# Kernel optimization log

Measured on AMD Instinct MI355X. Metric: run time of the kernel, lower is better.

## Reference

```python
import jax, jax.numpy as jnp
import numpy as np

B = 8          # batch_size
N = 2048       # N_particles
D_SP = 2       # spatial dims
D = 16         # D_SP + hidden_dim
K = 32         # max_num_neighbors
R = 0.08       # neighbor_radius
DT = 0.01      # leapfrog step
BIG = 1e9


def setup_inputs() -> dict:
    key = jax.random.key(0)
    ks = jax.random.split(key, 8)
    H, C = 64, 32
    # node state: small random hidden features, deterministic disk positions
    x = jax.random.normal(ks[0], (B * N, D), dtype=jnp.float32) * 0.001
    i = jnp.arange(N, dtype=jnp.float32)
    golden = jnp.pi * (3.0 - jnp.sqrt(5.0))
    theta = i * golden
    r = 0.6 * jnp.sqrt((i + 0.5) / N)
    pos = jnp.stack([r * jnp.cos(theta), r * jnp.sin(theta)], axis=1)  # [N,2]
    pos = jnp.tile(pos, (B, 1)) + 0.01 * jax.random.normal(ks[1], (B * N, 2), dtype=jnp.float32)
    x = x.at[:, :D_SP].set(pos)
    W1 = jax.random.normal(ks[2], (2 * D, H), dtype=jnp.float32) * (1.0 / np.sqrt(2 * D))
    b1 = jnp.zeros((H,), jnp.float32)
    W2 = jax.random.normal(ks[3], (H, C), dtype=jnp.float32) * (1.0 / np.sqrt(H))
    b2 = jnp.zeros((C,), jnp.float32)
    Wout = jax.random.normal(ks[4], (C, 1), dtype=jnp.float32) * (1.0 / np.sqrt(C))
    bout = jnp.zeros((1,), jnp.float32)
    batch = jnp.repeat(jnp.arange(B, dtype=jnp.int64), N)
    return {"x": x, "W1": W1, "b1": b1, "W2": W2, "b2": b2,
            "Wout": Wout, "bout": bout, "batch": batch, "steps": 2}


def reference(x, W1, b1, W2, b2, Wout, bout, batch, steps):
    Bn, Df = x.shape
    Bc = int(np.asarray(batch)[-1]) + 1      # batch is contiguous blocks
    Nn = Bn // Bc
    eye = jnp.eye(Nn, dtype=x.dtype) * BIG   # no self-loops (loop=False)

    def hamiltonian(xv):
        xb = xv.reshape(Bc, Nn, Df)
        pos = xb[:, :, :D_SP]                              # [B,N,2]
        # radius_graph: pairwise sq-dist per simulation, capped at K neighbors
        d2 = jnp.sum((pos[:, :, None, :] - pos[:, None, :, :]) ** 2, axis=-1)  # [B,N,N]
        d2 = d2 + eye
        negd, idx = jax.lax.top_k(-d2, K)                  # K nearest per node
        valid = (-negd) < (R * R)                          # [B,N,K]
        # gather neighbor states (HNNConv message on concat(x_i, x_j))
        xj = xb[jnp.arange(Bc)[:, None, None], idx]        # [B,N,K,D]
        xi = jnp.broadcast_to(xb[:, :, None, :], xj.shape)
        m = jnp.tanh(jnp.concatenate([xi, xj], axis=-1) @ W1 + b1)  # [B,N,K,H]
        m = m @ W2 + b2                                    # [B,N,K,C]
        m = jnp.where(valid[..., None], m, 0.0)
        agg = m.sum(axis=2)                                # sum aggregation [B,N,C]
        h = agg @ Wout + bout                              # per-node Hamiltonian [B,N,1]
        return h.sum()

    for _ in range(int(steps)):
        dHdx = jax.grad(hamiltonian)(x)
        x = x - DT * dHdx
    return x
```

## Files before the change

### kernel.cpp

```cpp
#include <hip/hip_runtime.h>
#include <cstdint>
#include <cstddef>

#define BB   8
#define NN   2048
#define DD   16
#define HHH  64
#define KK   32
#define CAP  96
#define FCAP 48
#define DT_C 0.01f
#define R2_C (0.08f * 0.08f)
#define CEXP (-2.885390081777927f)

#define BANDS    18
#define BAND_OFF 0.72f
#define BAND_INV 12.5f

#define WPB   8
#define BLOCK (WPB * 64)

__device__ __forceinline__ float dist2(float px, float py, float qx, float qy) {
    float dx = __fsub_rn(px, qx);
    float dy = __fsub_rn(py, qy);
    return __fadd_rn(__fmul_rn(dx, dx), __fmul_rn(dy, dy));
}

__device__ __forceinline__ int prefix_cnt(unsigned long long m) {
    return (int)__builtin_amdgcn_mbcnt_hi(
        (unsigned)(m >> 32), __builtin_amdgcn_mbcnt_lo((unsigned)m, 0u));
}

__device__ __forceinline__ int swizzled_particle(int blk, int w, int& bbase) {
    int vb = blk & 7, vi = blk >> 3;
    bbase = vb << 11;
    return bbase + vi * WPB + w;
}

template <bool FIRST>
__global__ __launch_bounds__(1024) void k_bin(
    const float* __restrict__ x, const float* __restrict__ pos,
    const float* __restrict__ W2, const float* __restrict__ Wout,
    float2* __restrict__ sortedPos, unsigned short* __restrict__ sortedIdx,
    int* __restrict__ bandStart, float* __restrict__ vOut) {
    __shared__ int hist[BANDS], base[BANDS + 1], cursor[BANDS];
    int bat = blockIdx.x;
    int bbase = bat << 11;
    int tid = threadIdx.x;
    if (tid < BANDS) hist[tid] = 0;
    if (blockIdx.x == 0 && tid >= 64 && tid < 64 + HHH) {
        int hh = tid - 64;
        float acc = 0.f;
        for (int c = 0; c < 32; c++) acc = fmaf(W2[hh * 32 + c], Wout[c], acc);
        vOut[hh] = acc;
    }
    __syncthreads();
    float2 q[2]; int bd[2];
#pragma unroll
    for (int u = 0; u < 2; ++u) {
        int i = tid + (u << 10);
        float2 qq;
        if (FIRST) qq = *(const float2*)(x + (size_t)(bbase + i) * DD);
        else       qq = *(const float2*)(pos + (size_t)(bbase + i) * 2);
        q[u] = qq;
        int band = (int)((qq.y + BAND_OFF) * BAND_INV);
        band = band < 0 ? 0 : (band > BANDS - 1 ? BANDS - 1 : band);
        bd[u] = band;
        atomicAdd(&hist[band], 1);
    }
    __syncthreads();
    if (tid == 0) {
        int acc = 0;
        for (int k = 0; k < BANDS; ++k) { base[k] = acc; cursor[k] = acc; acc += hist[k]; }
        base[BANDS] = acc;
    }
    __syncthreads();
    if (tid <= BANDS) bandStart[bat * 32 + tid] = base[tid];
#pragma unroll
    for (int u = 0; u < 2; ++u) {
        int i = tid + (u << 10);
        int dst = atomicAdd(&cursor[bd[u]], 1);
        sortedPos[bbase + dst] = q[u];
        sortedIdx[bbase + dst] = (unsigned short)i;
    }
}

__global__ __launch_bounds__(BLOCK) void k_neighbors(
    const float* __restrict__ x,
    const float2* __restrict__ sortedPos, const unsigned short* __restrict__ sortedIdx,
    const int* __restrict__ bandStart, const float* __restrict__ W1,
    float2* __restrict__ candList, unsigned short* __restrict__ fwdList,
    int* __restrict__ cntArr, float* __restrict__ cutArr,
    float* __restrict__ Aplane, float* __restrict__ Dplane) {
    __shared__ float2 sDJ[WPB][CAP];

    int tid = threadIdx.x;
    int w = tid >> 6, lane = tid & 63;
    int bbase;
    int p = swizzled_particle(blockIdx.x, w, bbase);
    int pl = p & (NN - 1);
    int bat = bbase >> 11;

    float xv = (lane < DD) ? x[(size_t)p * DD + lane] : 0.f;
    float px = __shfl(xv, 0), py = __shfl(xv, 1);
    float A = 0.f, Dv = 0.f;
#pragma unroll
    for (int f = 0; f < DD; f++) {
        float xf = __shfl(xv, f);
        A  = fmaf(xf, W1[f * HHH + lane], A);
        Dv = fmaf(xf, W1[(DD + f) * HHH + lane], Dv);
    }
    Aplane[((size_t)p << 6) + lane] = A;
    Dplane[((size_t)p << 6) + lane] = Dv;

    int bb = (int)((py + BAND_OFF) * BAND_INV);
    bb = bb < 0 ? 0 : (bb > BANDS - 1 ? BANDS - 1 : bb);
    int lo = bandStart[bat * 32 + (bb > 0 ? bb - 1 : 0)];
    int hi = bandStart[bat * 32 + (bb < BANDS - 1 ? bb + 2 : BANDS)];

    int cnt = 0;
    for (int c0 = lo; c0 < hi; c0 += 64) {
        int j = c0 + lane;
        float2 q = (j < hi) ? sortedPos[bbase + j] : make_float2(1e30f, 1e30f);
        float d2 = dist2(px, py, q.x, q.y);
        bool hit = (j < hi) && (d2 < R2_C);
        unsigned long long m = __ballot(hit);
        int idx = cnt + prefix_cnt(m);
        if (hit && idx < CAP)
            sDJ[w][idx] = make_float2(d2, __uint_as_float((unsigned)j));
        cnt += (int)__popcll(m);
    }
    if (cnt > CAP) cnt = CAP;
    __threadfence_block();

    float cutoff = R2_C;
    if (cnt > KK + 1) {
        const float INF = 1e30f;
        if (cnt <= 64) {
            float v = (lane < cnt) ? sDJ[w][lane].x : INF;
#pragma unroll
            for (int k = 2; k <= 64; k <<= 1) {
#pragma unroll
                for (int j = k >> 1; j > 0; j >>= 1) {
                    float pv = __shfl_xor(v, j);
                    bool up = ((lane & k) == 0);
                    bool takeMin = (((lane & j) == 0) == up);
                    v = takeMin ? fminf(v, pv) : fmaxf(v, pv);
                }
            }
            cutoff = __shfl(v, KK);
        } else {
            float e0 = (lane < cnt) ? sDJ[w][lane].x : INF;
            float e1 = (lane + 64 < cnt) ? sDJ[w][lane + 64].x : INF;
            int r0 = 0, q0 = 0, r1 = 0, q1 = 0;
            for (int k = 0; k < cnt; k++) {
                float val = sDJ[w][k].x;
                r0 += (val < e0); q0 += (val == e0);
                r1 += (val < e1); q1 += (val == e1);
            }
            bool c0 = (r0 <= KK) && (r0 + q0 > KK);
            bool c1 = (r1 <= KK) && (r1 + q1 > KK);
            float cand = c0 ? e0 : (c1 ? e1 : INF);
#pragma unroll
            for (int off = 32; off; off >>= 1) cand = fminf(cand, __shfl_xor(cand, off));
            cutoff = cand;
        }
    }

    int me = 0, mf = 0;
    for (int c0 = 0; c0 < cnt; c0 += 64) {
        int c = c0 + lane;
        bool act = c < cnt;
        float2 e = sDJ[w][act ? c : 0];
        unsigned js = __float_as_uint(e.y);
        int jo = act ? (int)sortedIdx[bbase + js] : pl;
        bool keep = act && (jo != pl);
        unsigned long long mK = __ballot(keep);
        int ie = me + prefix_cnt(mK);
        if (keep)
            candList[(size_t)p * CAP + ie] = make_float2(e.x, __uint_as_float((unsigned)jo));
        me += (int)__popcll(mK);
        bool fw = keep && (e.x <= cutoff);
        unsigned long long mF = __ballot(fw);
        int iF = mf + prefix_cnt(mF);
        if (fw && iF < FCAP) fwdList[(size_t)p * FCAP + iF] = (unsigned short)jo;
        mf += (int)__popcll(mF);
    }
    if (mf > FCAP) mf = FCAP;
    if (lane == 0) { cutArr[p] = cutoff; cntArr[p] = me | (mf << 16); }
}

__global__ __launch_bounds__(BLOCK) void k_grad(
    const float* __restrict__ x,
    const float* __restrict__ cutArr, const int* __restrict__ cntArr,
    const float2* __restrict__ candList, const unsigned short* __restrict__ fwdList,
    const float* __restrict__ Aplane, const float* __restrict__ Dplane,
    const float* __restrict__ W1, const float* __restrict__ b1,
    const float* __restrict__ vArr,
    float* __restrict__ xOut, float* __restrict__ posOut) {
    __shared__ float sW1t[HHH * 33];
    __shared__ alignas(16) unsigned short sFwd[WPB][FCAP];
    __shared__ alignas(16) unsigned short sRev[WPB][CAP];
    __shared__ float sS[WPB][128];

    int tid = threadIdx.x;
    int w = tid >> 6, h = tid & 63;
    int bbase;
    int p = swizzled_particle(blockIdx.x, w, bbase);

    for (int t = tid; t < 2 * DD * HHH; t += BLOCK) {
        int f = t >> 6, hh = t & 63;
        sW1t[hh * 33 + f] = W1[t];
    }
    __syncthreads();

    float b1h = b1[h];
    float Apb = Aplane[((size_t)p << 6) + h] + b1h;
    float Dpb = Dplane[((size_t)p << 6) + h] + b1h;
    float vh4 = 4.f * vArr[h];
    int packed = cntArr[p];
    int cnt = packed & 0xffff;
    int mf = packed >> 16;

    if (h < mf) sFwd[w][h] = fwdList[(size_t)p * FCAP + h];

    int mr = 0;
    for (int c0 = 0; c0 < cnt; c0 += 64) {
        int c = c0 + h;
        bool act = c < cnt;
        float2 e = candList[(size_t)p * CAP + (act ? c : 0)];
        unsigned jl = __float_as_uint(e.y) & (NN - 1);
        bool rev = act && (e.x <= cutArr[bbase + jl]);
        unsigned long long mR = __ballot(rev);
        int iR = mr + prefix_cnt(mR);
        if (rev) sRev[w][iR] = (unsigned short)jl;
        mr += (int)__popcll(mR);
    }
    __threadfence_block();

    const float* baseD = Dplane + ((size_t)bbase << 6);
    const float* baseA = Aplane + ((size_t)bbase << 6);
    float T1 = 0.f, T2 = 0.f;

    auto s2core = [&](float z) {
        float a = __builtin_amdgcn_exp2f(CEXP * fabsf(z));
        float bb = 1.f + a;
        return a * __builtin_amdgcn_rcpf(bb * bb);
    };

#define UNPACK8(Q0, Q1, U)                                            \
    unsigned U[8];                                                    \
    U[0] = (unsigned)__builtin_amdgcn_readfirstlane(Q0.x);            \
    U[1] = (unsigned)__builtin_amdgcn_readfirstlane(Q0.y);            \
    U[2] = (unsigned)__builtin_amdgcn_readfirstlane(Q0.z);            \
    U[3] = (unsigned)__builtin_amdgcn_readfirstlane(Q0.w);            \
    U[4] = (unsigned)__builtin_amdgcn_readfirstlane(Q1.x);            \
    U[5] = (unsigned)__builtin_amdgcn_readfirstlane(Q1.y);            \
    U[6] = (unsigned)__builtin_amdgcn_readfirstlane(Q1.z);            \
    U[7] = (unsigned)__builtin_amdgcn_readfirstlane(Q1.w);

    {
        const unsigned short* L = sFwd[w];
        int c = 0;
        for (; c + 16 <= mf; c += 16) {
            int4 q0 = *(const int4*)(L + c);
            int4 q1 = *(const int4*)(L + c + 8);
            UNPACK8(q0, q1, u)
            float d[16];
#pragma unroll
            for (int k = 0; k < 8; ++k) {
                d[2 * k]     = baseD[((size_t)(u[k] & 0xffffu) << 6) + h];
                d[2 * k + 1] = baseD[((size_t)(u[k] >> 16) << 6) + h];
            }
#pragma unroll
            for (int k = 0; k < 16; ++k) T1 += s2core(Apb + d[k]);
        }
        for (; c + 8 <= mf; c += 8) {
            int4 q0 = *(const int4*)(L + c);
            int4 q1 = q0;
            UNPACK8(q0, q1, u)
            float d[8];
#pragma unroll
            for (int k = 0; k < 4; ++k) {
                d[2 * k]     = baseD[((size_t)(u[k] & 0xffffu) << 6) + h];
                d[2 * k + 1] = baseD[((size_t)(u[k] >> 16) << 6) + h];
            }
#pragma unroll
            for (int k = 0; k < 8; ++k) T1 += s2core(Apb + d[k]);
        }
        for (; c < mf; ++c) {
            unsigned jl = (unsigned)__builtin_amdgcn_readfirstlane((int)L[c]);
            T1 += s2core(Apb + baseD[((size_t)jl << 6) + h]);
        }
    }
    {
        const unsigned short* L = sRev[w];
        int c = 0;
        for (; c + 16 <= mr; c += 16) {
            int4 q0 = *(const int4*)(L + c);
            int4 q1 = *(const int4*)(L + c + 8);
            UNPACK8(q0, q1, u)
            float d[16];
#pragma unroll
            for (int k = 0; k < 8; ++k) {
                d[2 * k]     = baseA[((size_t)(u[k] & 0xffffu) << 6) + h];
                d[2 * k + 1] = baseA[((size_t)(u[k] >> 16) << 6) + h];
            }
#pragma unroll
            for (int k = 0; k < 16; ++k) T2 += s2core(Dpb + d[k]);
        }
        for (; c + 8 <= mr; c += 8) {
            int4 q0 = *(const int4*)(L + c);
            int4 q1 = q0;
            UNPACK8(q0, q1, u)
            float d[8];
#pragma unroll
            for (int k = 0; k < 4; ++k) {
                d[2 * k]     = baseA[((size_t)(u[k] & 0xffffu) << 6) + h];
                d[2 * k + 1] = baseA[((size_t)(u[k] >> 16) << 6) + h];
            }
#pragma unroll
            for (int k = 0; k < 8; ++k) T2 += s2core(Dpb + d[k]);
        }
        for (; c < mr; ++c) {
            unsigned jl = (unsigned)__builtin_amdgcn_readfirstlane((int)L[c]);
            T2 += s2core(Dpb + baseA[((size_t)jl << 6) + h]);
        }
    }
#undef UNPACK8

    sS[w][h] = vh4 * T1;
    sS[w][64 + h] = vh4 * T2;
    __threadfence_block();

    float g = 0.f;
    if (h < 32) {
        const float* Sv = &sS[w][(h < 16) ? 0 : 64];
        float a0 = 0.f, a1 = 0.f, a2 = 0.f, a3 = 0.f;
        for (int hh = 0; hh < 64; hh += 4) {
            a0 = fmaf(sW1t[(hh + 0) * 33 + h], Sv[hh + 0], a0);
            a1 = fmaf(sW1t[(hh + 1) * 33 + h], Sv[hh + 1], a1);
            a2 = fmaf(sW1t[(hh + 2) * 33 + h], Sv[hh + 2], a2);
            a3 = fmaf(sW1t[(hh + 3) * 33 + h], Sv[hh + 3], a3);
        }
        g = (a0 + a1) + (a2 + a3);
    }
    float g2 = __shfl(g, (h + 16) & 63);
    if (h < DD) {
        float xn = x[(size_t)p * DD + h] - DT_C * (g + g2);
        xOut[(size_t)p * DD + h] = xn;
        if (h < 2) posOut[p * 2 + h] = xn;
    }
}

extern "C" void kernel_launch(void* const* d_in, const int* in_sizes, int n_in,
                              void* d_out, int out_size, void* d_ws, size_t ws_size,
                              hipStream_t stream) {
    const float* x0   = (const float*)d_in[0];
    const float* W1   = (const float*)d_in[1];
    const float* b1   = (const float*)d_in[2];
    const float* W2   = (const float*)d_in[3];
    const float* Wout = (const float*)d_in[5];
    float* out = (float*)d_out;

    float* ws   = (float*)d_ws;
    float* posA = ws;
    float* posB = posA + 32768;
    float* x1   = posB + 32768;
    float* Apl  = x1 + 262144;
    float* Dpl  = Apl + 16384 * 64;
    float* cut  = Dpl + 16384 * 64;
    int*   cnt  = (int*)(cut + 16384);
    float2* cand = (float2*)(cnt + 16384);
    unsigned short* fwd = (unsigned short*)(cand + (size_t)16384 * CAP);
    float2* sPosS = (float2*)(fwd + (size_t)16384 * FCAP);
    unsigned short* sIdx = (unsigned short*)(sPosS + 16384);
    int* bandStart = (int*)(sIdx + 16384);
    float* vArr = (float*)(bandStart + 8 * 32);

    const int NB = (BB * NN) / WPB;

    k_bin<true><<<BB, 1024, 0, stream>>>(x0, nullptr, W2, Wout, sPosS, sIdx,
                                         bandStart, vArr);
    k_neighbors<<<NB, BLOCK, 0, stream>>>(x0, sPosS, sIdx, bandStart, W1,
                                          cand, fwd, cnt, cut, Apl, Dpl);
    k_grad<<<NB, BLOCK, 0, stream>>>(x0, cut, cnt, cand, fwd, Apl, Dpl,
                                     W1, b1, vArr, x1, posB);
    k_bin<false><<<BB, 1024, 0, stream>>>(nullptr, posB, W2, Wout, sPosS, sIdx,
                                          bandStart, vArr);
    k_neighbors<<<NB, BLOCK, 0, stream>>>(x1, sPosS, sIdx, bandStart, W1,
                                          cand, fwd, cnt, cut, Apl, Dpl);
    k_grad<<<NB, BLOCK, 0, stream>>>(x1, cut, cnt, cand, fwd, Apl, Dpl,
                                     W1, b1, vArr, out, posA);
}
```

Baseline: 170.7 us.

## Replace 1D band binning with 2D cell grid and process particles in sorted order

The neighbor search now bins particles into a 17x17 uniform 2D grid instead of horizontal bands. Each particle scans only the three row-contiguous ranges covering its 3x3 cell neighborhood, which cuts the number of candidate distance tests. The cell histogram prefix sum becomes a warp-level scan. Per-particle work is also indexed by cell-sorted slot, so candidate and forward lists hold sorted indices and gathers of Aplane, Dplane and cutArr in the gradient kernel are spatially local. The cost is an extra sortedIdx indirection when reading x and writing the outputs, and a more complex candidate-index computation.

```diff
diff --git a/kernel.cpp b/kernel.cpp
--- a/kernel.cpp
+++ b/kernel.cpp
@@ -13,9 +13,11 @@
 #define R2_C (0.08f * 0.08f)
 #define CEXP (-2.885390081777927f)
 
-#define BANDS    18
-#define BAND_OFF 0.72f
-#define BAND_INV 12.5f
+#define GRID 17
+#define NCEL (GRID * GRID)
+#define GOFF 0.68f
+#define CINV 12.5f
+#define CSTRIDE 320
 
 #define WPB   8
 #define BLOCK (WPB * 64)
@@ -31,10 +33,13 @@
         (unsigned)(m >> 32), __builtin_amdgcn_mbcnt_lo((unsigned)m, 0u));
 }
 
-__device__ __forceinline__ int swizzled_particle(int blk, int w, int& bbase) {
-    int vb = blk & 7, vi = blk >> 3;
-    bbase = vb << 11;
-    return bbase + vi * WPB + w;
+__device__ __forceinline__ int swizzled_slot(int blk, int w, int& bbase) {
+    bbase = (blk & 7) << 11;
+    return (blk >> 3) * WPB + w;
+}
+
+__device__ __forceinline__ int clampi(int v, int lo, int hi) {
+    return v < lo ? lo : (v > hi ? hi : v);
 }
 
 template <bool FIRST>
@@ -42,53 +47,68 @@
     const float* __restrict__ x, const float* __restrict__ pos,
     const float* __restrict__ W2, const float* __restrict__ Wout,
     float2* __restrict__ sortedPos, unsigned short* __restrict__ sortedIdx,
-    int* __restrict__ bandStart, float* __restrict__ vOut) {
-    __shared__ int hist[BANDS], base[BANDS + 1], cursor[BANDS];
-    int bat = blockIdx.x;
-    int bbase = bat << 11;
-    int tid = threadIdx.x;
-    if (tid < BANDS) hist[tid] = 0;
-    if (blockIdx.x == 0 && tid >= 64 && tid < 64 + HHH) {
-        int hh = tid - 64;
+    int* __restrict__ cellStart, float* __restrict__ vOut) {
+    __shared__ int hist[NCEL], base[NCEL + 1], cursor[NCEL];
+    int bat = blockIdx.x, bbase = bat << 11, tid = threadIdx.x;
+    if (tid < NCEL) hist[tid] = 0;
+    if (blockIdx.x == 0 && tid >= 512 && tid < 512 + HHH) {
+        int hh = tid - 512;
         float acc = 0.f;
         for (int c = 0; c < 32; c++) acc = fmaf(W2[hh * 32 + c], Wout[c], acc);
         vOut[hh] = acc;
     }
     __syncthreads();
-    float2 q[2]; int bd[2];
+    float2 q[2]; int cid[2];
 #pragma unroll
     for (int u = 0; u < 2; ++u) {
         int i = tid + (u << 10);
-        float2 qq;
-        if (FIRST) qq = *(const float2*)(x + (size_t)(bbase + i) * DD);
-        else       qq = *(const float2*)(pos + (size_t)(bbase + i) * 2);
+        float2 qq = FIRST ? *(const float2*)(x + (size_t)(bbase + i) * DD)
+                          : *(const float2*)(pos + (size_t)(bbase + i) * 2);
         q[u] = qq;
-        int band = (int)((qq.y + BAND_OFF) * BAND_INV);
-        band = band < 0 ? 0 : (band > BANDS - 1 ? BANDS - 1 : band);
-        bd[u] = band;
-        atomicAdd(&hist[band], 1);
+        int cx = clampi((int)((qq.x + GOFF) * CINV), 0, GRID - 1);
+        int cy = clampi((int)((qq.y + GOFF) * CINV), 0, GRID - 1);
+        cid[u] = cy * GRID + cx;
+        atomicAdd(&hist[cid[u]], 1);
     }
     __syncthreads();
-    if (tid == 0) {
-        int acc = 0;
-        for (int k = 0; k < BANDS; ++k) { base[k] = acc; cursor[k] = acc; acc += hist[k]; }
-        base[BANDS] = acc;
+    if (tid < 64) {
+        int loc[5], s = 0;
+#pragma unroll
+        for (int k = 0; k < 5; ++k) {
+            int idx = tid * 5 + k;
+            loc[k] = (idx < NCEL) ? hist[idx] : 0;
+            s += loc[k];
+        }
+        int pre = s;
+#pragma unroll
+        for (int off = 1; off < 64; off <<= 1) {
+            int t = __shfl_up(pre, off);
+            if (tid >= off) pre += t;
+        }
+        pre -= s;
+#pragma unroll
+        for (int k = 0; k < 5; ++k) {
+            int idx = tid * 5 + k;
+            if (idx <= NCEL) base[idx] = pre;
+            pre += loc[k];
+        }
     }
     __syncthreads();
-    if (tid <= BANDS) bandStart[bat * 32 + tid] = base[tid];
+    if (tid < NCEL) cursor[tid] = base[tid];
+    if (tid <= NCEL) cellStart[bat * CSTRIDE + tid] = base[tid];
+    __syncthreads();
 #pragma unroll
     for (int u = 0; u < 2; ++u) {
-        int i = tid + (u << 10);
-        int dst = atomicAdd(&cursor[bd[u]], 1);
+        int dst = atomicAdd(&cursor[cid[u]], 1);
         sortedPos[bbase + dst] = q[u];
-        sortedIdx[bbase + dst] = (unsigned short)i;
+        sortedIdx[bbase + dst] = (unsigned short)(tid + (u << 10));
     }
 }
 
 __global__ __launch_bounds__(BLOCK) void k_neighbors(
     const float* __restrict__ x,
     const float2* __restrict__ sortedPos, const unsigned short* __restrict__ sortedIdx,
-    const int* __restrict__ bandStart, const float* __restrict__ W1,
+    const int* __restrict__ cellStart, const float* __restrict__ W1,
     float2* __restrict__ candList, unsigned short* __restrict__ fwdList,
     int* __restrict__ cntArr, float* __restrict__ cutArr,
     float* __restrict__ Aplane, float* __restrict__ Dplane) {
@@ -97,11 +117,13 @@
     int tid = threadIdx.x;
     int w = tid >> 6, lane = tid & 63;
     int bbase;
-    int p = swizzled_particle(blockIdx.x, w, bbase);
-    int pl = p & (NN - 1);
+    int s = swizzled_slot(blockIdx.x, w, bbase);
     int bat = bbase >> 11;
-
-    float xv = (lane < DD) ? x[(size_t)p * DD + lane] : 0.f;
+    int gs = bbase + s;
+
+    int jol = (int)sortedIdx[gs];
+    const float* xrow = x + (size_t)(bbase + jol) * DD;
+    float xv = (lane < DD) ? xrow[lane] : 0.f;
     float px = __shfl(xv, 0), py = __shfl(xv, 1);
     float A = 0.f, Dv = 0.f;
 #pragma unroll
@@ -110,20 +132,41 @@
         A  = fmaf(xf, W1[f * HHH + lane], A);
         Dv = fmaf(xf, W1[(DD + f) * HHH + lane], Dv);
     }
-    Aplane[((size_t)p << 6) + lane] = A;
-    Dplane[((size_t)p << 6) + lane] = Dv;
-
-    int bb = (int)((py + BAND_OFF) * BAND_INV);
-    bb = bb < 0 ? 0 : (bb > BANDS - 1 ? BANDS - 1 : bb);
-    int lo = bandStart[bat * 32 + (bb > 0 ? bb - 1 : 0)];
-    int hi = bandStart[bat * 32 + (bb < BANDS - 1 ? bb + 2 : BANDS)];
+    Aplane[((size_t)gs << 6) + lane] = A;
+    Dplane[((size_t)gs << 6) + lane] = Dv;
+
+    const int* CS = cellStart + bat * CSTRIDE;
+    int cx = clampi((int)((px + GOFF) * CINV), 0, GRID - 1);
+    int cy = clampi((int)((py + GOFF) * CINV), 0, GRID - 1);
+    int xlo = cx > 0 ? cx - 1 : 0;
+    int xhi = cx < GRID - 1 ? cx + 1 : GRID - 1;
+    int rs0 = 0, rl0 = 0, rs1 = 0, rl1 = 0, rs2 = 0, rl2 = 0;
+    if (cy > 0) {
+        int a = CS[(cy - 1) * GRID + xlo], b = CS[(cy - 1) * GRID + xhi + 1];
+        rs0 = a; rl0 = b - a;
+    }
+    {
+        int a = CS[cy * GRID + xlo], b = CS[cy * GRID + xhi + 1];
+        rs1 = a; rl1 = b - a;
+    }
+    if (cy < GRID - 1) {
+        int a = CS[(cy + 1) * GRID + xlo], b = CS[(cy + 1) * GRID + xhi + 1];
+        rs2 = a; rl2 = b - a;
+    }
+    int tot = rl0 + rl1 + rl2;
 
     int cnt = 0;
-    for (int c0 = lo; c0 < hi; c0 += 64) {
-        int j = c0 + lane;
-        float2 q = (j < hi) ? sortedPos[bbase + j] : make_float2(1e30f, 1e30f);
+    for (int c0 = 0; c0 < tot; c0 += 64) {
+        int t = c0 + lane;
+        int j = rs0 + t;
+        int u1 = t - rl0;
+        if (u1 >= 0) j = rs1 + u1;
+        int u2 = u1 - rl1;
+        if (u2 >= 0) j = rs2 + u2;
+        bool in = t < tot;
+        float2 q = sortedPos[bbase + (in ? j : 0)];
         float d2 = dist2(px, py, q.x, q.y);
-        bool hit = (j < hi) && (d2 < R2_C);
+        bool hit = in && (d2 < R2_C);
         unsigned long long m = __ballot(hit);
         int idx = cnt + prefix_cnt(m);
         if (hit && idx < CAP)
@@ -173,25 +216,23 @@
         bool act = c < cnt;
         float2 e = sDJ[w][act ? c : 0];
         unsigned js = __float_as_uint(e.y);
-        int jo = act ? (int)sortedIdx[bbase + js] : pl;
-        bool keep = act && (jo != pl);
+        bool keep = act && ((int)js != s);
         unsigned long long mK = __ballot(keep);
         int ie = me + prefix_cnt(mK);
-        if (keep)
-            candList[(size_t)p * CAP + ie] = make_float2(e.x, __uint_as_float((unsigned)jo));
+        if (keep) candList[(size_t)gs * CAP + ie] = e;
         me += (int)__popcll(mK);
         bool fw = keep && (e.x <= cutoff);
         unsigned long long mF = __ballot(fw);
         int iF = mf + prefix_cnt(mF);
-        if (fw && iF < FCAP) fwdList[(size_t)p * FCAP + iF] = (unsigned short)jo;
+        if (fw && iF < FCAP) fwdList[(size_t)gs * FCAP + iF] = (unsigned short)js;
         mf += (int)__popcll(mF);
     }
     if (mf > FCAP) mf = FCAP;
-    if (lane == 0) { cutArr[p] = cutoff; cntArr[p] = me | (mf << 16); }
+    if (lane == 0) { cutArr[gs] = cutoff; cntArr[gs] = me | (mf << 16); }
 }
 
 __global__ __launch_bounds__(BLOCK) void k_grad(
-    const float* __restrict__ x,
+    const float* __restrict__ x, const unsigned short* __restrict__ sortedIdx,
     const float* __restrict__ cutArr, const int* __restrict__ cntArr,
     const float2* __restrict__ candList, const unsigned short* __restrict__ fwdList,
     const float* __restrict__ Aplane, const float* __restrict__ Dplane,
@@ -206,7 +247,8 @@
     int tid = threadIdx.x;
     int w = tid >> 6, h = tid & 63;
     int bbase;
-    int p = swizzled_particle(blockIdx.x, w, bbase);
+    int s = swizzled_slot(blockIdx.x, w, bbase);
+    int gs = bbase + s;
 
     for (int t = tid; t < 2 * DD * HHH; t += BLOCK) {
         int f = t >> 6, hh = t & 63;
@@ -215,20 +257,20 @@
     __syncthreads();
 
     float b1h = b1[h];
-    float Apb = Aplane[((size_t)p << 6) + h] + b1h;
-    float Dpb = Dplane[((size_t)p << 6) + h] + b1h;
+    float Apb = Aplane[((size_t)gs << 6) + h] + b1h;
+    float Dpb = Dplane[((size_t)gs << 6) + h] + b1h;
     float vh4 = 4.f * vArr[h];
-    int packed = cntArr[p];
+    int packed = cntArr[gs];
     int cnt = packed & 0xffff;
     int mf = packed >> 16;
 
-    if (h < mf) sFwd[w][h] = fwdList[(size_t)p * FCAP + h];
+    if (h < mf) sFwd[w][h] = fwdList[(size_t)gs * FCAP + h];
 
     int mr = 0;
     for (int c0 = 0; c0 < cnt; c0 += 64) {
         int c = c0 + h;
         bool act = c < cnt;
-        float2 e = candList[(size_t)p * CAP + (act ? c : 0)];
+        float2 e = candList[(size_t)gs * CAP + (act ? c : 0)];
         unsigned jl = __float_as_uint(e.y) & (NN - 1);
         bool rev = act && (e.x <= cutArr[bbase + jl]);
         unsigned long long mR = __ballot(rev);
@@ -346,10 +388,12 @@
         g = (a0 + a1) + (a2 + a3);
     }
     float g2 = __shfl(g, (h + 16) & 63);
+    int jo = (int)sortedIdx[gs];
     if (h < DD) {
-        float xn = x[(size_t)p * DD + h] - DT_C * (g + g2);
-        xOut[(size_t)p * DD + h] = xn;
-        if (h < 2) posOut[p * 2 + h] = xn;
+        size_t prow = (size_t)(bbase + jo) * DD;
+        float xn = x[prow + h] - DT_C * (g + g2);
+        xOut[prow + h] = xn;
+        if (h < 2) posOut[(bbase + jo) * 2 + h] = xn;
     }
 }
 
@@ -375,21 +419,21 @@
     unsigned short* fwd = (unsigned short*)(cand + (size_t)16384 * CAP);
     float2* sPosS = (float2*)(fwd + (size_t)16384 * FCAP);
     unsigned short* sIdx = (unsigned short*)(sPosS + 16384);
-    int* bandStart = (int*)(sIdx + 16384);
-    float* vArr = (float*)(bandStart + 8 * 32);
+    int* cellStart = (int*)(sIdx + 16384);
+    float* vArr = (float*)(cellStart + BB * CSTRIDE);
 
     const int NB = (BB * NN) / WPB;
 
     k_bin<true><<<BB, 1024, 0, stream>>>(x0, nullptr, W2, Wout, sPosS, sIdx,
-                                         bandStart, vArr);
-    k_neighbors<<<NB, BLOCK, 0, stream>>>(x0, sPosS, sIdx, bandStart, W1,
+                                         cellStart, vArr);
+    k_neighbors<<<NB, BLOCK, 0, stream>>>(x0, sPosS, sIdx, cellStart, W1,
                                           cand, fwd, cnt, cut, Apl, Dpl);
-    k_grad<<<NB, BLOCK, 0, stream>>>(x0, cut, cnt, cand, fwd, Apl, Dpl,
+    k_grad<<<NB, BLOCK, 0, stream>>>(x0, sIdx, cut, cnt, cand, fwd, Apl, Dpl,
                                      W1, b1, vArr, x1, posB);
     k_bin<false><<<BB, 1024, 0, stream>>>(nullptr, posB, W2, Wout, sPosS, sIdx,
-                                          bandStart, vArr);
-    k_neighbors<<<NB, BLOCK, 0, stream>>>(x1, sPosS, sIdx, bandStart, W1,
+                                          cellStart, vArr);
+    k_neighbors<<<NB, BLOCK, 0, stream>>>(x1, sPosS, sIdx, cellStart, W1,
                                           cand, fwd, cnt, cut, Apl, Dpl);
-    k_grad<<<NB, BLOCK, 0, stream>>>(x1, cut, cnt, cand, fwd, Apl, Dpl,
+    k_grad<<<NB, BLOCK, 0, stream>>>(x1, sIdx, cut, cnt, cand, fwd, Apl, Dpl,
                                      W1, b1, vArr, out, posA);
 }
```

Measured after the change: 167.4 us. About the same (-1.9%).
